# Optimization experiments

Measured on AMD Instinct MI355X. Metric: run time of the kernel, lower is better.

Reference implementation:

```python
import jax, jax.numpy as jnp
import numpy as np

EPS = 1e-5
N_LANG = 5

def _ln(x, gamma, beta):
    mu = jnp.mean(x, axis=-1, keepdims=True)
    var = jnp.mean((x - mu) ** 2, axis=-1, keepdims=True)
    return (x - mu) * jax.lax.rsqrt(var + EPS) * gamma + beta

def setup_inputs() -> dict:
    key = jax.random.key(0)
    ks = jax.random.split(key, 20)
    B, S, E, T, H = 16, 512, 768, 768, 1024
    s = lambda fan_in: 1.0 / np.sqrt(fan_in)
    inp = {
        'ner_features': jax.random.normal(ks[0], (B, S, E), jnp.float32),
        'topic_features': jax.random.normal(ks[1], (B, S, T), jnp.float32),
        'language_ids': jax.random.randint(ks[2], (B,), 0, N_LANG, jnp.int64),
        # ner transform: Linear(E,H) + LayerNorm(H)
        'W_ner': jax.random.uniform(ks[3], (E, H), jnp.float32, -s(E), s(E)),
        'b_ner': jnp.zeros((H,), jnp.float32),
        'g_ner': jnp.ones((H,), jnp.float32),
        'be_ner': jnp.zeros((H,), jnp.float32),
        # topic transform: Linear(T,H) + LayerNorm(H)
        'W_top': jax.random.uniform(ks[4], (T, H), jnp.float32, -s(T), s(T)),
        'b_top': jnp.zeros((H,), jnp.float32),
        'g_top': jnp.ones((H,), jnp.float32),
        'be_top': jnp.zeros((H,), jnp.float32),
        # 5 language gate networks, stacked on leading lang axis
        'Wg1': jax.random.uniform(ks[5], (N_LANG, 2 * H, H), jnp.float32, -s(2 * H), s(2 * H)),
        'bg1': jnp.zeros((N_LANG, H), jnp.float32),
        'gg': jnp.ones((N_LANG, H), jnp.float32),
        'bg': jnp.zeros((N_LANG, H), jnp.float32),
        'Wg2': jax.random.uniform(ks[6], (N_LANG, H, 2), jnp.float32, -s(H), s(H)),
        'bg2': jnp.zeros((N_LANG, 2), jnp.float32),
    }
    return inp

def reference(ner_features, topic_features, language_ids,
              W_ner, b_ner, g_ner, be_ner,
              W_top, b_top, g_top, be_top,
              Wg1, bg1, gg, bg, Wg2, bg2):
    # shared transforms: [B,S,H]
    ner_t = jax.nn.relu(_ln(ner_features @ W_ner + b_ner, g_ner, be_ner))
    top_t = jax.nn.relu(_ln(topic_features @ W_top + b_top, g_top, be_top))
    combined = jnp.concatenate([ner_t, top_t], axis=-1)  # [B,S,2H]
    # all-language gate MLPs (faithful to the original redundant compute)
    h = jnp.einsum('bsd,ldh->lbsh', combined, Wg1) + bg1[:, None, None, :]
    h = jax.nn.relu(_ln(h, gg[:, None, None, :], bg[:, None, None, :]))
    gates_all = jax.nn.sigmoid(jnp.einsum('lbsh,lhk->lbsk', h, Wg2) + bg2[:, None, None, :])  # [L,B,S,2]
    mask = (language_ids[None, :] == jnp.arange(N_LANG)[:, None]).astype(gates_all.dtype)  # [L,B]
    gates = jnp.einsum('lb,lbsk->bsk', mask, gates_all)  # [B,S,2]
    gated_ner = ner_t * gates[..., 0:1]
    gated_topic = top_t * gates[..., 1:2]
    # dropout in eval mode (identity) for determinism
    return gated_ner, gated_topic
```

## Files before the change

### kernel.cpp

```cpp
#include <hip/hip_runtime.h>

typedef __attribute__((ext_vector_type(8))) short short8;
typedef __attribute__((ext_vector_type(4))) float f32x4;

__device__ __forceinline__ float bf2f(unsigned short u) {
    union { unsigned int i; float f; } v; v.i = ((unsigned int)u) << 16; return v.f;
}
__device__ __forceinline__ unsigned short f2bf(float f) {
    union { float f; unsigned int i; } v; v.f = f;
    unsigned int r = v.i + 0x7fffu + ((v.i >> 16) & 1u);
    return (unsigned short)(r >> 16);
}
__device__ __forceinline__ void gload16(const unsigned short* g, unsigned short* l) {
    __builtin_amdgcn_global_load_lds(
        (const __attribute__((address_space(1))) unsigned int*)g,
        (__attribute__((address_space(3))) unsigned int*)l, 16, 0, 0);
}

template<int K, int MODE>
__global__ __launch_bounds__(512, 2) void gemm8(
    const unsigned short* __restrict__ A,
    const unsigned short* __restrict__ Bta,
    const unsigned short* __restrict__ Btb,
    const float* __restrict__ biasa,
    const float* __restrict__ biasb,
    unsigned short* __restrict__ Cb,
    const int* __restrict__ lang)
{
    constexpr int BN   = (MODE == 0) ? 256 : 128;
    constexpr int NBLK = 1024 / BN;
    constexpr int NT   = K / 64;
    constexpr int NPH  = (MODE == 0) ? 4 : 2;
    constexpr int MPP  = 8 / NPH;
    constexpr int NR   = (MODE == 0) ? 4 : 2;
    constexpr int WNS  = BN / 4;
    constexpr int VN   = (MODE == 0) ? 6 : 4;

    __shared__ __align__(16) unsigned short As[2][256][64];
    __shared__ __align__(16) unsigned short Bs[2][BN][64];

    const int t = threadIdx.x;
    const int nwg = gridDim.x;
    const int bid = blockIdx.x;
    const int swz = (bid & 7) * (nwg >> 3) + (bid >> 3);
    const int gm0 = (swz / NBLK) * 256;
    const int gn0 = (swz % NBLK) * BN;

    const unsigned short* Bt;
    const float* bias;
    int sel = 0;
    if (MODE == 0) {
        sel = gm0 >> 13;
        Bt = sel ? Btb : Bta;
        bias = sel ? biasb : biasa;
    } else {
        const int l = lang[gm0 >> 9];
        Bt = Bta + (size_t)l * ((size_t)K * 1024);
        bias = biasa + l * 1024;
    }

    const int lane = t & 63, w = t >> 6;
    const int wm = w >> 2, wn = w & 3;
    const int fr = lane & 15, g4 = lane >> 4, f7 = lane & 7;

    const int sr  = t >> 3;
    const int gsw = ((t & 7) ^ (sr & 7)) * 8;
    const int lc  = (t & 7) * 8;
    const unsigned short* agb = A  + (size_t)(gm0 + sr) * K + gsw;
    const unsigned short* bgb = Bt + (size_t)(gn0 + sr) * K + gsw;

    f32x4 acc[8][NR];
#pragma unroll
    for (int m = 0; m < 8; ++m)
#pragma unroll
        for (int n = 0; n < NR; ++n)
            acc[m][n] = (f32x4){0.f, 0.f, 0.f, 0.f};

    auto stA = [&](int buf, int h, int kb) {
#pragma unroll
        for (int j = 0; j < 2; ++j)
            gload16(agb + (size_t)(j * 128 + h * 64) * K + kb,
                    &As[buf][h * 128 + j * 64 + sr][lc]);
    };
    auto stB = [&](int buf, int h, int kb) {
#pragma unroll
        for (int j = 0; j < 2; ++j)
            gload16(bgb + (size_t)(h * 128 + j * 64) * K + kb,
                    &Bs[buf][h * 128 + j * 64 + sr][lc]);
    };

#define RDA(Q)                                                                \
    _Pragma("unroll")                                                         \
    for (int i = 0; i < MPP; ++i) {                                           \
        const int mf = (Q) * MPP + i;                                         \
        const int row = (mf >> 2) * 128 + wm * 64 + (mf & 3) * 16 + fr;       \
        _Pragma("unroll")                                                     \
        for (int kk = 0; kk < 2; ++kk)                                        \
            af_[i][kk] = *(const short8*)&As[c][row][((kk * 4 + g4) ^ f7) * 8];\
    }

#define RDB()                                                                 \
    _Pragma("unroll")                                                         \
    for (int n = 0; n < NR; ++n) {                                            \
        const int row = wn * WNS + n * 16 + fr;                               \
        _Pragma("unroll")                                                     \
        for (int kk = 0; kk < 2; ++kk)                                        \
            bf_[n][kk] = *(const short8*)&Bs[c][row][((kk * 4 + g4) ^ f7) * 8];\
    }

#define MFMA16(Q)                                                             \
    __builtin_amdgcn_s_setprio(1);                                            \
    _Pragma("unroll")                                                         \
    for (int kk = 0; kk < 2; ++kk)                                            \
        _Pragma("unroll")                                                     \
        for (int i = 0; i < MPP; ++i)                                         \
            _Pragma("unroll")                                                 \
            for (int n = 0; n < NR; ++n)                                      \
                acc[(Q) * MPP + i][n] = __builtin_amdgcn_mfma_f32_16x16x32_bf16(\
                    af_[i][kk], bf_[n][kk], acc[(Q) * MPP + i][n], 0, 0, 0);  \
    __builtin_amdgcn_s_setprio(0);

#define PH_TOP()  __builtin_amdgcn_sched_barrier(0); __builtin_amdgcn_s_barrier(); \
                  asm volatile("s_waitcnt lgkmcnt(0)" ::: "memory");               \
                  __builtin_amdgcn_sched_barrier(0);
#define PH_BOT()  __builtin_amdgcn_sched_barrier(0); __builtin_amdgcn_s_barrier();

    if (MODE == 0) {
        stB(0, 0, 0); stB(0, 1, 0); stA(0, 0, 0); stA(0, 1, 0);
        stB(1, 0, 64); stB(1, 1, 64); stA(1, 0, 64);
        asm volatile("s_waitcnt vmcnt(6)" ::: "memory");
    } else {
        stB(0, 0, 0); stA(0, 0, 0); stA(0, 1, 0);
        stB(1, 0, 64); stA(1, 0, 64);
        asm volatile("s_waitcnt vmcnt(4)" ::: "memory");
    }
    __builtin_amdgcn_s_barrier();

#pragma unroll 2
    for (int u = 0; u < NT; ++u) {
        const int c = u & 1;
        const int kb1 = (u + 1) * 64, kb2 = (u + 2) * 64;
        const bool s1 = (u + 1 < NT), s2 = (u + 2 < NT);
        short8 bf_[NR][2], af_[MPP][2];

        RDB();
        RDA(0);
        if (s1) stA(c ^ 1, 1, kb1);
        PH_TOP();
        MFMA16(0);
        PH_BOT();

        if (MODE == 0) {
            RDA(1);
            if (s2) stB(c, 0, kb2);
            PH_TOP();
            MFMA16(1);
            PH_BOT();
            RDA(2);
            if (s2) stB(c, 1, kb2);
            PH_TOP();
            MFMA16(2);
            PH_BOT();
            RDA(3);
            if (s2) stA(c, 0, kb2);
            if (s2) asm volatile("s_waitcnt vmcnt(%0)" :: "i"(VN) : "memory");
            else    asm volatile("s_waitcnt vmcnt(0)" ::: "memory");
            PH_TOP();
            MFMA16(3);
            PH_BOT();
        } else {
            RDA(1);
            if (s2) { stB(c, 0, kb2); stA(c, 0, kb2); }
            if (s2) asm volatile("s_waitcnt vmcnt(%0)" :: "i"(VN) : "memory");
            else    asm volatile("s_waitcnt vmcnt(0)" ::: "memory");
            PH_TOP();
            MFMA16(1);
            PH_BOT();
        }
    }

    const int fq = lane >> 4;
    const size_t pitch  = (MODE == 0) ? 2048 : 1024;
    const size_t coloff = (MODE == 0) ? (size_t)sel * 1024 : 0;
    const int rbase = (MODE == 0) ? (gm0 & 8191) : gm0;
#pragma unroll
    for (int n = 0; n < NR; ++n) {
        const int col = gn0 + wn * WNS + n * 16 + fr;
        const float bv = bias[col];
#pragma unroll
        for (int m = 0; m < 8; ++m) {
            const int row0 = rbase + wm * 128 + m * 16 + fq * 4;
#pragma unroll
            for (int r = 0; r < 4; ++r)
                Cb[(size_t)(row0 + r) * pitch + coloff + col] = f2bf(acc[m][n][r] + bv);
        }
    }
#undef RDA
#undef RDB
#undef MFMA16
#undef PH_TOP
#undef PH_BOT
}

__global__ __launch_bounds__(256) void wt_bf16(
    const float* __restrict__ W, unsigned short* __restrict__ Wt, int K, int N)
{
    __shared__ float tile[32][33];
    W  += (size_t)blockIdx.z * K * N;
    Wt += (size_t)blockIdx.z * K * N;
    const int n0 = blockIdx.x * 32, k0 = blockIdx.y * 32;
    const int x = threadIdx.x & 31, y = threadIdx.x >> 5;
#pragma unroll
    for (int i = 0; i < 4; ++i)
        tile[y + 8 * i][x] = W[(size_t)(k0 + y + 8 * i) * N + n0 + x];
    __syncthreads();
#pragma unroll
    for (int i = 0; i < 4; ++i)
        Wt[(size_t)(n0 + y + 8 * i) * K + k0 + x] = f2bf(tile[x][y + 8 * i]);
}

__global__ __launch_bounds__(256) void conv_bf16(
    const float* __restrict__ in, unsigned short* __restrict__ out)
{
    const size_t i = ((size_t)blockIdx.x * 256 + threadIdx.x) * 8;
    const float4 a = ((const float4*)(in + i))[0];
    const float4 b = ((const float4*)(in + i))[1];
    ushort4 u, v;
    u.x = f2bf(a.x); u.y = f2bf(a.y); u.z = f2bf(a.z); u.w = f2bf(a.w);
    v.x = f2bf(b.x); v.y = f2bf(b.y); v.z = f2bf(b.z); v.w = f2bf(b.w);
    *(ushort4*)(out + i)     = u;
    *(ushort4*)(out + i + 4) = v;
}

__global__ __launch_bounds__(256) void ln_relu_c(
    unsigned short* __restrict__ comb,
    const float* __restrict__ gn, const float* __restrict__ bn,
    const float* __restrict__ gt, const float* __restrict__ btp)
{
    const int b = blockIdx.x, t = threadIdx.x;
    const int r = b >> 1, half = b & 1;
    unsigned short* p = comb + (size_t)r * 2048 + half * 1024 + t * 4;
    ushort4 u = *(const ushort4*)p;
    const float x0 = bf2f(u.x), x1 = bf2f(u.y), x2 = bf2f(u.z), x3 = bf2f(u.w);
    float s1 = x0 + x1 + x2 + x3;
    float s2 = x0 * x0 + x1 * x1 + x2 * x2 + x3 * x3;
#pragma unroll
    for (int off = 32; off > 0; off >>= 1) {
        s1 += __shfl_down(s1, off);
        s2 += __shfl_down(s2, off);
    }
    __shared__ float red[8];
    const int wid = t >> 6;
    if ((t & 63) == 0) { red[wid] = s1; red[4 + wid] = s2; }
    __syncthreads();
    s1 = red[0] + red[1] + red[2] + red[3];
    s2 = red[4] + red[5] + red[6] + red[7];
    const float mean = s1 * (1.0f / 1024.0f);
    const float var = fmaxf(s2 * (1.0f / 1024.0f) - mean * mean, 0.0f);
    const float rstd = rsqrtf(var + 1e-5f);
    const float* G  = half ? gt : gn;
    const float* Be = half ? btp : bn;
    const float4 g  = ((const float4*)G)[t];
    const float4 be = ((const float4*)Be)[t];
    u.x = f2bf(fmaxf((x0 - mean) * rstd * g.x + be.x, 0.0f));
    u.y = f2bf(fmaxf((x1 - mean) * rstd * g.y + be.y, 0.0f));
    u.z = f2bf(fmaxf((x2 - mean) * rstd * g.z + be.z, 0.0f));
    u.w = f2bf(fmaxf((x3 - mean) * rstd * g.w + be.w, 0.0f));
    *(ushort4*)p = u;
}

__global__ __launch_bounds__(256) void ln_gate(
    const unsigned short* __restrict__ preln, const unsigned short* __restrict__ comb,
    const float* __restrict__ gg, const float* __restrict__ bgb,
    const float* __restrict__ Wg2, const float* __restrict__ bg2,
    const int* __restrict__ lang,
    float* __restrict__ outN, float* __restrict__ outT)
{
    const int r = blockIdx.x, t = threadIdx.x;
    const int l = lang[r >> 9];
    const ushort4 u = *(const ushort4*)(preln + (size_t)r * 1024 + t * 4);
    const float x0 = bf2f(u.x), x1 = bf2f(u.y), x2 = bf2f(u.z), x3 = bf2f(u.w);
    float s1 = x0 + x1 + x2 + x3;
    float s2 = x0 * x0 + x1 * x1 + x2 * x2 + x3 * x3;
#pragma unroll
    for (int off = 32; off > 0; off >>= 1) {
        s1 += __shfl_down(s1, off);
        s2 += __shfl_down(s2, off);
    }
    __shared__ float red[8];
    const int wid = t >> 6;
    if ((t & 63) == 0) { red[wid] = s1; red[4 + wid] = s2; }
    __syncthreads();
    s1 = red[0] + red[1] + red[2] + red[3];
    s2 = red[4] + red[5] + red[6] + red[7];
    const float mean = s1 * (1.0f / 1024.0f);
    const float var = fmaxf(s2 * (1.0f / 1024.0f) - mean * mean, 0.0f);
    const float rstd = rsqrtf(var + 1e-5f);
    const float4 g  = ((const float4*)(gg + l * 1024))[t];
    const float4 be = ((const float4*)(bgb + l * 1024))[t];
    const float h0 = fmaxf((x0 - mean) * rstd * g.x + be.x, 0.0f);
    const float h1 = fmaxf((x1 - mean) * rstd * g.y + be.y, 0.0f);
    const float h2 = fmaxf((x2 - mean) * rstd * g.z + be.z, 0.0f);
    const float h3 = fmaxf((x3 - mean) * rstd * g.w + be.w, 0.0f);
    const float4* W = (const float4*)(Wg2 + (size_t)l * 2048);
    const float4 wa = W[t * 2], wb = W[t * 2 + 1];
    float d0 = h0 * wa.x + h1 * wa.z + h2 * wb.x + h3 * wb.z;
    float d1 = h0 * wa.y + h1 * wa.w + h2 * wb.y + h3 * wb.w;
#pragma unroll
    for (int off = 32; off > 0; off >>= 1) {
        d0 += __shfl_down(d0, off);
        d1 += __shfl_down(d1, off);
    }
    __syncthreads();
    if ((t & 63) == 0) { red[wid] = d0; red[4 + wid] = d1; }
    __syncthreads();
    d0 = red[0] + red[1] + red[2] + red[3] + bg2[l * 2 + 0];
    d1 = red[4] + red[5] + red[6] + red[7] + bg2[l * 2 + 1];
    const float g0 = 1.0f / (1.0f + __expf(-d0));
    const float g1 = 1.0f / (1.0f + __expf(-d1));
    const ushort4 cn = *(const ushort4*)(comb + (size_t)r * 2048 + t * 4);
    const ushort4 ct = *(const ushort4*)(comb + (size_t)r * 2048 + 1024 + t * 4);
    float4 a, b;
    a.x = bf2f(cn.x) * g0; a.y = bf2f(cn.y) * g0; a.z = bf2f(cn.z) * g0; a.w = bf2f(cn.w) * g0;
    b.x = bf2f(ct.x) * g1; b.y = bf2f(ct.y) * g1; b.z = bf2f(ct.z) * g1; b.w = bf2f(ct.w) * g1;
    ((float4*)(outN + (size_t)r * 1024))[t] = a;
    ((float4*)(outT + (size_t)r * 1024))[t] = b;
}

extern "C" void kernel_launch(void* const* d_in, const int* in_sizes, int n_in,
                              void* d_out, int out_size, void* d_ws, size_t ws_size,
                              hipStream_t stream)
{
    const float* ner    = (const float*)d_in[0];
    const float* top    = (const float*)d_in[1];
    const int*   lang   = (const int*)d_in[2];
    const float* W_ner  = (const float*)d_in[3];
    const float* b_ner  = (const float*)d_in[4];
    const float* g_ner  = (const float*)d_in[5];
    const float* be_ner = (const float*)d_in[6];
    const float* W_top  = (const float*)d_in[7];
    const float* b_top  = (const float*)d_in[8];
    const float* g_top  = (const float*)d_in[9];
    const float* be_top = (const float*)d_in[10];
    const float* Wg1    = (const float*)d_in[11];
    const float* bg1    = (const float*)d_in[12];
    const float* gg     = (const float*)d_in[13];
    const float* bgb    = (const float*)d_in[14];
    const float* Wg2    = (const float*)d_in[15];
    const float* bg2    = (const float*)d_in[16];

    float* out  = (float*)d_out;
    float* outN = out;
    float* outT = out + 8388608;

    char* ws = (char*)d_ws;
    unsigned short* combined = (unsigned short*)ws;
    unsigned short* actb     = (unsigned short*)(ws + 33554432);
    unsigned short* preln2   = (unsigned short*)(ws + 33554432);
    unsigned short* Wg1t     = (unsigned short*)(ws + 58720256);
    unsigned short* W_nert   = (unsigned short*)outT;
    unsigned short* W_topt   = W_nert + 786432;

    wt_bf16<<<dim3(32, 24, 1), 256, 0, stream>>>(W_ner, W_nert, 768, 1024);
    wt_bf16<<<dim3(32, 24, 1), 256, 0, stream>>>(W_top, W_topt, 768, 1024);
    wt_bf16<<<dim3(32, 64, 5), 256, 0, stream>>>(Wg1, Wg1t, 2048, 1024);

    conv_bf16<<<3072, 256, 0, stream>>>(ner, actb);
    conv_bf16<<<3072, 256, 0, stream>>>(top, actb + 6291456);

    gemm8<768, 0><<<256, 512, 0, stream>>>(
        actb, W_nert, W_topt, b_ner, b_top, combined, nullptr);
    ln_relu_c<<<16384, 256, 0, stream>>>(combined, g_ner, be_ner, g_top, be_top);

    gemm8<2048, 1><<<256, 512, 0, stream>>>(
        combined, Wg1t, nullptr, bg1, nullptr, preln2, lang);

    ln_gate<<<8192, 256, 0, stream>>>(preln2, combined, gg, bgb, Wg2, bg2, lang, outN, outT);
}
```

Baseline: 148.8 us.

## Double-buffer A fragments so LDS reads overlap MFMA phases in GEMM loop

Restructures the GEMM main loop so each phase issues its MFMA block first and then reads the next phase's A fragments from LDS into an alternate register set (ping-pong afP/afQ). B and the first A fragments for the next k-tile are prefetched at the end of the previous iteration. Global-load waitcnt values are re-tuned to match the new issue order. The aim is to hide LDS read latency behind matrix-core work, at the cost of extra fragment registers and more intricate vmcnt bookkeeping.

Result: slower. 154.2 us (+3.6%).

```diff
diff --git a/kernel.cpp b/kernel.cpp
--- a/kernel.cpp
+++ b/kernel.cpp
@@ -34,7 +34,6 @@
     constexpr int MPP  = 8 / NPH;
     constexpr int NR   = (MODE == 0) ? 4 : 2;
     constexpr int WNS  = BN / 4;
-    constexpr int VN   = (MODE == 0) ? 6 : 4;
 
     __shared__ __align__(16) unsigned short As[2][256][64];
     __shared__ __align__(16) unsigned short Bs[2][BN][64];
@@ -89,92 +88,95 @@
                     &Bs[buf][h * 128 + j * 64 + sr][lc]);
     };
 
-#define RDA(Q)                                                                \
-    _Pragma("unroll")                                                         \
-    for (int i = 0; i < MPP; ++i) {                                           \
-        const int mf = (Q) * MPP + i;                                         \
-        const int row = (mf >> 2) * 128 + wm * 64 + (mf & 3) * 16 + fr;       \
-        _Pragma("unroll")                                                     \
-        for (int kk = 0; kk < 2; ++kk)                                        \
-            af_[i][kk] = *(const short8*)&As[c][row][((kk * 4 + g4) ^ f7) * 8];\
-    }
-
-#define RDB()                                                                 \
-    _Pragma("unroll")                                                         \
-    for (int n = 0; n < NR; ++n) {                                            \
-        const int row = wn * WNS + n * 16 + fr;                               \
-        _Pragma("unroll")                                                     \
-        for (int kk = 0; kk < 2; ++kk)                                        \
-            bf_[n][kk] = *(const short8*)&Bs[c][row][((kk * 4 + g4) ^ f7) * 8];\
-    }
-
-#define MFMA16(Q)                                                             \
-    __builtin_amdgcn_s_setprio(1);                                            \
-    _Pragma("unroll")                                                         \
-    for (int kk = 0; kk < 2; ++kk)                                            \
-        _Pragma("unroll")                                                     \
-        for (int i = 0; i < MPP; ++i)                                         \
-            _Pragma("unroll")                                                 \
-            for (int n = 0; n < NR; ++n)                                      \
+    short8 afP[MPP][2], afQ[MPP][2], bf_[NR][2];
+
+#define RDA(Q, AF, BUF)                                                        \
+    _Pragma("unroll")                                                          \
+    for (int i = 0; i < MPP; ++i) {                                            \
+        const int mf = (Q) * MPP + i;                                          \
+        const int row = (mf >> 2) * 128 + wm * 64 + (mf & 3) * 16 + fr;        \
+        _Pragma("unroll")                                                      \
+        for (int kk = 0; kk < 2; ++kk)                                         \
+            AF[i][kk] = *(const short8*)&As[BUF][row][((kk * 4 + g4) ^ f7) * 8];\
+    }
+#define RDB(BUF)                                                               \
+    _Pragma("unroll")                                                          \
+    for (int n = 0; n < NR; ++n) {                                             \
+        const int row = wn * WNS + n * 16 + fr;                                \
+        _Pragma("unroll")                                                      \
+        for (int kk = 0; kk < 2; ++kk)                                         \
+            bf_[n][kk] = *(const short8*)&Bs[BUF][row][((kk * 4 + g4) ^ f7) * 8];\
+    }
+#define MFMA16(Q, AF)                                                          \
+    __builtin_amdgcn_s_setprio(1);                                             \
+    _Pragma("unroll")                                                          \
+    for (int kk = 0; kk < 2; ++kk)                                             \
+        _Pragma("unroll")                                                      \
+        for (int i = 0; i < MPP; ++i)                                          \
+            _Pragma("unroll")                                                  \
+            for (int n = 0; n < NR; ++n)                                       \
                 acc[(Q) * MPP + i][n] = __builtin_amdgcn_mfma_f32_16x16x32_bf16(\
-                    af_[i][kk], bf_[n][kk], acc[(Q) * MPP + i][n], 0, 0, 0);  \
+                    AF[i][kk], bf_[n][kk], acc[(Q) * MPP + i][n], 0, 0, 0);    \
     __builtin_amdgcn_s_setprio(0);
-
-#define PH_TOP()  __builtin_amdgcn_sched_barrier(0); __builtin_amdgcn_s_barrier(); \
-                  asm volatile("s_waitcnt lgkmcnt(0)" ::: "memory");               \
-                  __builtin_amdgcn_sched_barrier(0);
-#define PH_BOT()  __builtin_amdgcn_sched_barrier(0); __builtin_amdgcn_s_barrier();
+#define VM(n) asm volatile("s_waitcnt vmcnt(%0)" :: "i"(n) : "memory")
+#define PH_TOP() __builtin_amdgcn_sched_barrier(0); __builtin_amdgcn_s_barrier(); \
+                 asm volatile("s_waitcnt lgkmcnt(0)" ::: "memory");               \
+                 __builtin_amdgcn_sched_barrier(0)
+#define PH_BOT() __builtin_amdgcn_sched_barrier(0); __builtin_amdgcn_s_barrier()
 
     if (MODE == 0) {
         stB(0, 0, 0); stB(0, 1, 0); stA(0, 0, 0); stA(0, 1, 0);
         stB(1, 0, 64); stB(1, 1, 64); stA(1, 0, 64);
-        asm volatile("s_waitcnt vmcnt(6)" ::: "memory");
+        VM(6);
     } else {
         stB(0, 0, 0); stA(0, 0, 0); stA(0, 1, 0);
         stB(1, 0, 64); stA(1, 0, 64);
-        asm volatile("s_waitcnt vmcnt(4)" ::: "memory");
+        VM(4);
     }
     __builtin_amdgcn_s_barrier();
-
-#pragma unroll 2
+    RDB(0);
+    RDA(0, afP, 0);
+
     for (int u = 0; u < NT; ++u) {
-        const int c = u & 1;
+        const int c = u & 1, o = c ^ 1;
         const int kb1 = (u + 1) * 64, kb2 = (u + 2) * 64;
         const bool s1 = (u + 1 < NT), s2 = (u + 2 < NT);
-        short8 bf_[NR][2], af_[MPP][2];
-
-        RDB();
-        RDA(0);
-        if (s1) stA(c ^ 1, 1, kb1);
-        PH_TOP();
-        MFMA16(0);
-        PH_BOT();
 
         if (MODE == 0) {
-            RDA(1);
+            PH_TOP();
+            MFMA16(0, afP);
+            if (s1) stA(o, 1, kb1);
+            RDA(1, afQ, c);
+            if (s1) { VM(8); } else { VM(0); }
+            PH_BOT();
+            PH_TOP();
+            MFMA16(1, afQ);
             if (s2) stB(c, 0, kb2);
-            PH_TOP();
-            MFMA16(1);
-            PH_BOT();
-            RDA(2);
+            RDA(2, afP, c);
+            PH_BOT();
+            PH_TOP();
+            MFMA16(2, afP);
             if (s2) stB(c, 1, kb2);
-            PH_TOP();
-            MFMA16(2);
-            PH_BOT();
-            RDA(3);
+            RDA(3, afQ, c);
+            if (s2) { VM(6); } else if (s1) { VM(2); } else { VM(0); }
+            PH_BOT();
+            PH_TOP();
+            MFMA16(3, afQ);
             if (s2) stA(c, 0, kb2);
-            if (s2) asm volatile("s_waitcnt vmcnt(%0)" :: "i"(VN) : "memory");
-            else    asm volatile("s_waitcnt vmcnt(0)" ::: "memory");
-            PH_TOP();
-            MFMA16(3);
+            if (s1) { RDB(o); RDA(0, afP, o); }
             PH_BOT();
         } else {
-            RDA(1);
+            PH_TOP();
+            MFMA16(0, afP);
+            if (s1) stA(o, 1, kb1);
+            RDA(1, afQ, c);
+            if (s1) { VM(2); } else { VM(0); }
+            PH_BOT();
+            PH_TOP();
+            MFMA16(1, afQ);
             if (s2) { stB(c, 0, kb2); stA(c, 0, kb2); }
-            if (s2) asm volatile("s_waitcnt vmcnt(%0)" :: "i"(VN) : "memory");
-            else    asm volatile("s_waitcnt vmcnt(0)" ::: "memory");
-            PH_TOP();
-            MFMA16(1);
+            if (s1) { RDB(o); RDA(0, afP, o); }
+            if (s2) { VM(4); } else { VM(0); }
             PH_BOT();
         }
     }
@@ -198,6 +200,7 @@
 #undef RDA
 #undef RDB
 #undef MFMA16
+#undef VM
 #undef PH_TOP
 #undef PH_BOT
 }
```
